# Kernel tuning notes

Hardware: AMD Instinct MI355X
Metric: run time of the kernel (lower is better)

Reference implementation:

```python
import jax, jax.numpy as jnp
import numpy as np

E = 128          # embedding_dim
H = 128          # decoder_hidden_dim
N = 200000       # number of candidate nodes


def setup_inputs() -> dict:
    key = jax.random.key(0)
    k0, k1, k2, k3, k4, k5 = jax.random.split(key, 6)
    return {
        "current_node_emb": jax.random.normal(k0, (1, E), jnp.float32),
        "context_emb": jax.random.normal(k1, (1, E), jnp.float32),
        "candidate_node_embs": jax.random.normal(k2, (N, E), jnp.float32),
        "Wq": jax.random.normal(k3, (H, 2 * E), jnp.float32) * 0.05,  # nn.Linear(2E->H, bias=False) weight
        "Wk": jax.random.normal(k4, (H, E), jnp.float32) * 0.05,      # nn.Linear(E->H, bias=False) weight
        "mask": jax.random.randint(k5, (1, N), 0, 2, jnp.int32),
    }


def reference(current_node_emb, context_emb, candidate_node_embs, Wq, Wk, mask):
    # combined_input = cat([current, context], dim=1) -> [1, 2E]
    combined = jnp.concatenate([current_node_emb, context_emb], axis=1)
    query = combined @ Wq.T                      # [1, H]
    keys = candidate_node_embs @ Wk.T            # [N, H]
    attn_scores = query @ keys.T                 # [1, N]
    masked = jnp.where(mask == 0, -jnp.inf, attn_scores)
    probs = jax.nn.softmax(masked, axis=1)       # [1, N]

    n = probs.shape[1]
    k = min(50, max(1, int(0.5 * n)))            # static Python int -> jit-friendly
    top_probs, _ = jax.lax.top_k(probs, k)       # [1, k]
    threshold = top_probs[:, -1:]                # [1, 1]
    top_mask = probs >= threshold
    filtered = probs * top_mask
    filtered = filtered / (jnp.sum(filtered, axis=1, keepdims=True) + 1e-10)

    log_probs_all = jnp.log(filtered + 1e-10)    # [1, N]
    # Categorical(filtered): true-zero probability outside top-k
    logits = jnp.where(filtered > 0, jnp.log(filtered), -jnp.inf)
    action_idx = jax.random.categorical(jax.random.key(42), logits, axis=1)  # [1]
    log_prob_action = jnp.take_along_axis(logits, action_idx[:, None], axis=1)[:, 0]  # [1]
    return (log_probs_all, log_prob_action, action_idx)
```

## Files before the change

### kernel.cpp

```cpp
#include <hip/hip_runtime.h>
#include <math.h>


#define CAP 4096
#define MAXB 128
#define NEG_INF (-__builtin_inff())

__device__ __forceinline__ unsigned int f2ord(float f){
  unsigned int b = __float_as_uint(f);
  return (b & 0x80000000u) ? ~b : (b | 0x80000000u);
}
__device__ __forceinline__ unsigned int rotl32(unsigned int x, int d){
  return (x << d) | (x >> (32 - d));
}

__device__ float gumbel_from_idx(unsigned int idx){
  unsigned int x0 = 0u, x1 = idx;
  const unsigned int ks0 = 0u, ks1 = 42u;
  const unsigned int ks2 = 0u ^ 42u ^ 0x1BD11BDAu;
  x0 += ks0; x1 += ks1;
#define TF_RND(r) { x0 += x1; x1 = rotl32(x1, (r)); x1 ^= x0; }
  TF_RND(13) TF_RND(15) TF_RND(26) TF_RND(6)
  x0 += ks1; x1 += ks2 + 1u;
  TF_RND(17) TF_RND(29) TF_RND(16) TF_RND(24)
  x0 += ks2; x1 += ks0 + 2u;
  TF_RND(13) TF_RND(15) TF_RND(26) TF_RND(6)
  x0 += ks0; x1 += ks1 + 3u;
  TF_RND(17) TF_RND(29) TF_RND(16) TF_RND(24)
  x0 += ks1; x1 += ks2 + 4u;
  TF_RND(13) TF_RND(15) TF_RND(26) TF_RND(6)
  x0 += ks2; x1 += ks0 + 5u;
#undef TF_RND
  unsigned int bits = x0 ^ x1;
  unsigned int fb = (bits >> 9) | 0x3f800000u;
  float f = __uint_as_float(fb) - 1.0f;
  float u = (f < 1.17549435e-38f) ? 1.17549435e-38f : f;
  return -logf(-logf(u));
}

__global__ __launch_bounds__(256) void k_prep(const float* __restrict__ cur,
    const float* __restrict__ ctx, const float* __restrict__ Wq,
    const float* __restrict__ Wk, float* __restrict__ v,
    unsigned int* __restrict__ hist, unsigned int* __restrict__ scal_u){
  __shared__ float q[128];
  __shared__ float vpart[256];
  int t = threadIdx.x;
  int lane = t & 63, wave = t >> 6;
  int hl = lane & 31, hi = lane >> 5;
  for (int k = t; k < 2048; k += 256) hist[k] = 0u;
  if (t < 16) scal_u[t] = 0u;
  float4 cb0 = ((const float4*)cur)[hl];
  float4 cb1 = ((const float4*)ctx)[hl];
  const float4* Wq4 = (const float4*)Wq;
  #pragma unroll 4
  for (int i = 0; i < 16; ++i){
    int row = wave * 32 + 2 * i + hi;
    float4 w0 = Wq4[row * 64 + hl];
    float4 w1 = Wq4[row * 64 + 32 + hl];
    float d = fmaf(w0.x, cb0.x, fmaf(w0.y, cb0.y, fmaf(w0.z, cb0.z, w0.w * cb0.w)));
    d = fmaf(w1.x, cb1.x, fmaf(w1.y, cb1.y, fmaf(w1.z, cb1.z, fmaf(w1.w, cb1.w, d))));
    d += __shfl_xor(d, 1, 64);
    d += __shfl_xor(d, 2, 64);
    d += __shfl_xor(d, 4, 64);
    d += __shfl_xor(d, 8, 64);
    d += __shfl_xor(d, 16, 64);
    if (hl == 0) q[row] = d;
  }
  __syncthreads();
  int col = t & 127, half = t >> 7;
  const float* wkp = Wk + half * 64 * 128 + col;
  const float* qp  = q + half * 64;
  float acc = 0.f;
  #pragma unroll 8
  for (int h = 0; h < 64; ++h) acc = fmaf(qp[h], wkp[h * 128], acc);
  vpart[t] = acc;
  __syncthreads();
  if (t < 128) v[t] = vpart[t] + vpart[t + 128];
}

__global__ __launch_bounds__(256) void k_score(const float* __restrict__ cand,
    const int* __restrict__ mask, const float* __restrict__ v,
    float* __restrict__ scores, float* __restrict__ out, int N){
  const float NLOG = logf(1e-10f);
  int t = threadIdx.x;
  int lane = t & 63, wave = t >> 6;
  int hi = lane >> 5, hl = lane & 31;
  float4 v4 = ((const float4*)v)[hl];
  const float4* cp = (const float4*)cand;
  int base = (blockIdx.x * 4 + wave) * 16;
  int m[8];
  #pragma unroll
  for (int k = 0; k < 8; ++k){
    int r = base + 2 * k + hi;
    r = (r < N) ? r : (N - 1);
    m[k] = mask[r];
  }
  float4 c[8];
  #pragma unroll
  for (int k = 0; k < 8; ++k){
    int r = base + 2 * k + hi;
    r = (r < N) ? r : (N - 1);
    c[k] = make_float4(0.f, 0.f, 0.f, 0.f);
    if (m[k]) c[k] = cp[(size_t)r * 32 + hl];
  }
  float p[8];
  #pragma unroll
  for (int k = 0; k < 8; ++k)
    p[k] = fmaf(c[k].x, v4.x, fmaf(c[k].y, v4.y, fmaf(c[k].z, v4.z, c[k].w * v4.w)));
  #pragma unroll
  for (int k = 0; k < 8; ++k){
    p[k] += __shfl_xor(p[k], 1, 64);
    p[k] += __shfl_xor(p[k], 2, 64);
    p[k] += __shfl_xor(p[k], 4, 64);
    p[k] += __shfl_xor(p[k], 8, 64);
    p[k] += __shfl_xor(p[k], 16, 64);
  }
  float sv = p[0];
  #pragma unroll
  for (int k = 1; k < 8; ++k) sv = (hl == k) ? p[k] : sv;
  if (hl < 8){
    int r = base + 2 * hl + hi;
    int mm = (hl < 8) ? ((hl == 0) ? m[0] : 0) : 0; (void)mm;
    if (r < N) scores[r] = mask[r] ? sv : NEG_INF;
  }
  if (t < 16){
    int o4 = blockIdx.x * 16 + t;
    if (o4 * 4 + 3 < N){
      ((float4*)out)[o4] = make_float4(NLOG, NLOG, NLOG, NLOG);
    } else {
      #pragma unroll
      for (int e = 0; e < 4; ++e){ int i = o4 * 4 + e; if (i < N) out[i] = NLOG; }
    }
  }
}

__global__ __launch_bounds__(1024) void k_tail(const float* __restrict__ scores,
    unsigned int* __restrict__ scal_u, unsigned int* __restrict__ hist,
    float* __restrict__ zpart, unsigned int* __restrict__ cnt,
    unsigned int* __restrict__ buf_idx, float* __restrict__ buf_s,
    float* __restrict__ out, int N, int ktop, int nb){
  __shared__ float sch[4096];
  __shared__ unsigned int lh[2048];
  __shared__ unsigned int ich[4096];
  __shared__ unsigned int suf[256];
  __shared__ unsigned int cnt_l[MAXB], offs[MAXB];
  __shared__ float wred[16];
  __shared__ float rv[16], rl[16];
  __shared__ unsigned int ri[16];
  __shared__ float Z_sh, thr_sh, lnD_sh;
  __shared__ unsigned int u_lo_sh;
  __shared__ int csel_sh, pos_sh, C_sh;
  int t = threadIdx.x, b = blockIdx.x;
  int lane = t & 63, wave = t >> 6;
  for (int k = t; k < 2048; k += 1024) lh[k] = 0u;
  if (t == 0) pos_sh = 0;
  __syncthreads();
  int base = b * 4096;
  float ez = 0.f;
  {
    int i0 = base + 4 * t;
    float4 s4 = make_float4(NEG_INF, NEG_INF, NEG_INF, NEG_INF);
    if (i0 + 3 < N) s4 = ((const float4*)scores)[(base >> 2) + t];
    else {
      if (i0     < N) s4.x = scores[i0];
      if (i0 + 1 < N) s4.y = scores[i0 + 1];
      if (i0 + 2 < N) s4.z = scores[i0 + 2];
      if (i0 + 3 < N) s4.w = scores[i0 + 3];
    }
    sch[4 * t]     = s4.x;
    sch[4 * t + 1] = s4.y;
    sch[4 * t + 2] = s4.z;
    sch[4 * t + 3] = s4.w;
#define HVISIT(s_) { float sx = (s_); if (sx > NEG_INF){ \
    atomicAdd(&lh[f2ord(sx) >> 21], 1u); ez += expf(sx); } }
    HVISIT(s4.x) HVISIT(s4.y) HVISIT(s4.z) HVISIT(s4.w)
#undef HVISIT
  }
  #pragma unroll
  for (int off = 32; off; off >>= 1) ez += __shfl_xor(ez, off, 64);
  if (lane == 0) wred[wave] = ez;
  __syncthreads();
  for (int k = t; k < 2048; k += 1024){
    unsigned int cc = lh[k];
    if (cc) atomicAdd(&hist[k], cc);
  }
  __syncthreads();
  if (t == 0){
    float z = 0.f;
    for (int w = 0; w < 16; ++w) z += wred[w];
    zpart[b] = z;
    __threadfence();
    atomicAdd(&scal_u[8], 1u);
  }
  if (b == 0){
    if (t == 0){
      while (__hip_atomic_load(&scal_u[8], __ATOMIC_ACQUIRE, __HIP_MEMORY_SCOPE_AGENT)
             < (unsigned)nb) __builtin_amdgcn_s_sleep(2);
      csel_sh = -1;
    }
    __syncthreads();
    float z = (t < nb) ? zpart[t] : 0.f;
    if (t < 128){
      #pragma unroll
      for (int off = 32; off; off >>= 1) z += __shfl_xor(z, off, 64);
      if (lane == 0) wred[wave] = z;
    }
    if (t < 256){
      unsigned int csum = 0;
      #pragma unroll
      for (int k = 0; k < 8; ++k) csum += hist[t * 8 + k];
      suf[t] = csum;
    }
    __syncthreads();
    if (t == 0) Z_sh = wred[0] + wred[1];
    for (int d = 1; d < 256; d <<= 1){
      unsigned int add = 0u;
      if (t < 256 && t + d < 256) add = suf[t + d];
      __syncthreads();
      if (t < 256) suf[t] += add;
      __syncthreads();
    }
    if (t < 256){
      unsigned int st = suf[t];
      unsigned int sn = (t < 255) ? suf[t + 1] : 0u;
      if (st >= (unsigned)ktop && sn < (unsigned)ktop) csel_sh = t;
    }
    __syncthreads();
    if (t == 0){
      int b_sel = 0;
      if (csel_sh >= 0){
        int c = csel_sh;
        unsigned int cum = (c < 255) ? suf[c + 1] : 0u;
        for (int bi = 8 * c + 7; bi >= 8 * c; --bi){
          cum += hist[bi];
          if (cum >= (unsigned)ktop){ b_sel = bi; break; }
        }
      }
      u_lo_sh = ((unsigned int)b_sel) << 21;
      scal_u[5] = u_lo_sh;
      __threadfence();
      __hip_atomic_store(&scal_u[9], 1u, __ATOMIC_RELEASE, __HIP_MEMORY_SCOPE_AGENT);
    }
    __syncthreads();
  } else {
    if (t == 0){
      while (__hip_atomic_load(&scal_u[9], __ATOMIC_ACQUIRE, __HIP_MEMORY_SCOPE_AGENT)
             == 0u) __builtin_amdgcn_s_sleep(2);
      u_lo_sh = scal_u[5];
    }
    __syncthreads();
  }
  unsigned int u_lo = u_lo_sh;
  for (int j = t; j < 4096; j += 1024){
    float sx = sch[j];
    if (sx > NEG_INF && f2ord(sx) >= u_lo){
      int p = atomicAdd(&pos_sh, 1);
      if (p < 4096){
        buf_s[b * 4096 + p] = sx;
        buf_idx[b * 4096 + p] = (unsigned int)(base + j);
      }
    }
  }
  __syncthreads();
  if (t == 0){
    cnt[b] = (unsigned int)((pos_sh > 4096) ? 4096 : pos_sh);
    __threadfence();
    atomicAdd(&scal_u[10], 1u);
  }
  if (b != 0) return;
  if (t == 0){
    while (__hip_atomic_load(&scal_u[10], __ATOMIC_ACQUIRE, __HIP_MEMORY_SCOPE_AGENT)
           < (unsigned)nb) __builtin_amdgcn_s_sleep(2);
  }
  __syncthreads();
  float* s_lds = sch;
  unsigned int* i_lds = ich;
  if (t < nb) cnt_l[t] = cnt[t];
  if (t == 0) thr_sh = NEG_INF;
  __syncthreads();
  if (t == 0){
    unsigned int acc = 0;
    for (int b2 = 0; b2 < nb; ++b2){ offs[b2] = acc; acc += cnt_l[b2]; }
    C_sh = (acc > CAP) ? CAP : (int)acc;
  }
  __syncthreads();
  for (int b2 = 0; b2 < nb; ++b2){
    unsigned int cb = cnt_l[b2], ob = offs[b2];
    for (unsigned int j = t; j < cb; j += 1024){
      unsigned int p = ob + j;
      if (p < CAP){ s_lds[p] = buf_s[b2 * 4096 + j]; i_lds[p] = buf_idx[b2 * 4096 + j]; }
    }
  }
  __syncthreads();
  int C = C_sh;
  if (C > ktop){
    for (int j = t; j < C; j += 1024){
      float sj = s_lds[j];
      int g = 0, e = 0;
      for (int k2 = 0; k2 < C; ++k2){
        float sk = s_lds[k2];
        g += (sk > sj);
        e += (sk == sj);
      }
      if (g < ktop && g + e >= ktop) thr_sh = sj;
    }
  }
  __syncthreads();
  float s_thr = thr_sh;
  float part = 0.f;
  for (int j = t; j < C; j += 1024){
    float sj = s_lds[j];
    if (sj >= s_thr) part += expf(sj);
  }
  #pragma unroll
  for (int off = 32; off; off >>= 1) part += __shfl_xor(part, off, 64);
  if (lane == 0) wred[wave] = part;
  __syncthreads();
  if (t == 0){
    float T = 0.f;
    for (int w = 0; w < 16; ++w) T += wred[w];
    lnD_sh = logf(T + 1e-10f * Z_sh);
  }
  __syncthreads();
  float lnD = lnD_sh;
  for (int j = t; j < C; j += 1024){
    float sj = s_lds[j];
    if (sj >= s_thr) out[i_lds[j]] = logf(expf(sj - lnD) + 1e-10f);
  }
  float bestv = NEG_INF, bestlogit = NEG_INF;
  unsigned int bestidx = 0xFFFFFFFFu;
  for (int j = t; j < C; j += 1024){
    float sj = s_lds[j];
    if (sj >= s_thr){
      unsigned int idx = i_lds[j];
      float logit = sj - lnD;
      float val = logit + gumbel_from_idx(idx);
      if (val > bestv || (val == bestv && idx < bestidx)){
        bestv = val; bestlogit = logit; bestidx = idx;
      }
    }
  }
  #pragma unroll
  for (int off = 32; off; off >>= 1){
    float ov = __shfl_xor(bestv, off, 64);
    float ol = __shfl_xor(bestlogit, off, 64);
    unsigned int oi = (unsigned int)__shfl_xor((int)bestidx, off, 64);
    if (ov > bestv || (ov == bestv && oi < bestidx)){
      bestv = ov; bestlogit = ol; bestidx = oi;
    }
  }
  if (lane == 0){ rv[wave] = bestv; rl[wave] = bestlogit; ri[wave] = bestidx; }
  __syncthreads();
  if (t == 0){
    for (int w = 1; w < 16; ++w){
      if (rv[w] > rv[0] || (rv[w] == rv[0] && ri[w] < ri[0])){
        rv[0] = rv[w]; rl[0] = rl[w]; ri[0] = ri[w];
      }
    }
    out[N] = rl[0];
    out[N + 1] = (float)ri[0];
  }
}

extern "C" void kernel_launch(void* const* d_in, const int* in_sizes, int n_in,
                              void* d_out, int out_size, void* d_ws, size_t ws_size,
                              hipStream_t stream){
  const float* cur  = (const float*)d_in[0];
  const float* ctx  = (const float*)d_in[1];
  const float* cand = (const float*)d_in[2];
  const float* Wq   = (const float*)d_in[3];
  const float* Wk   = (const float*)d_in[4];
  const int*   mask = (const int*)d_in[5];
  int N = in_sizes[5];
  float* out = (float*)d_out;

  char* ws = (char*)d_ws;
  unsigned int* scal_u  = (unsigned int*)ws;
  float*        v       = (float*)(ws + 512);
  float*        zpart   = (float*)(ws + 1024);
  unsigned int* cnt     = (unsigned int*)(ws + 1536);
  unsigned int* hist    = (unsigned int*)(ws + 4096);
  float*        scores  = (float*)(ws + 16384);
  char*         bufbase = ws + 16384 + (((size_t)N * 4 + 255) & ~255ull);
  float*        buf_s   = (float*)bufbase;
  unsigned int* buf_idx = (unsigned int*)(bufbase + (size_t)MAXB * 4096 * 4);

  int ktop = N / 2; if (ktop < 1) ktop = 1; if (ktop > 50) ktop = 50;
  int g_score = (N + 63) / 64;
  int nb = (N + 4095) / 4096;
  if (nb > MAXB) nb = MAXB;

  k_prep<<<1, 256, 0, stream>>>(cur, ctx, Wq, Wk, v, hist, scal_u);
  k_score<<<g_score, 256, 0, stream>>>(cand, mask, v, scores, out, N);
  k_tail<<<nb, 1024, 0, stream>>>(scores, scal_u, hist, zpart, cnt,
                                  buf_idx, buf_s, out, N, ktop, nb);
}
```

Before: 220.8 us.

## Replace global histogram barrier with per-block selection and refined last-block filter

Each tail block now builds its own score histogram and keeps only its local top-k candidates. This removes the global histogram atomics and the two grid-wide spin-wait barriers. The last block to finish, found with an atomic counter, merges the per-block candidates and runs a second histogram pass to shrink the set before the quadratic rank-based threshold search. The scoring kernel now loads candidate rows unconditionally instead of waiting on the mask, which reads masked-out rows it previously skipped.

```diff
diff --git a/kernel.cpp b/kernel.cpp
--- a/kernel.cpp
+++ b/kernel.cpp
@@ -3,7 +3,9 @@
 
 
 #define CAP 4096
-#define MAXB 128
+#define SLOT 2048
+#define MAXB 64
+#define C2CAP 2048
 #define NEG_INF (-__builtin_inff())
 
 __device__ __forceinline__ unsigned int f2ord(float f){
@@ -38,16 +40,52 @@
   return -logf(-logf(u));
 }
 
+__device__ void hist_select(unsigned int* lh, unsigned int* suf, int* csel_sh,
+                            unsigned int* u_lo_sh, int ktop, int t){
+  if (t < 256){
+    unsigned int csum = 0;
+    #pragma unroll
+    for (int k = 0; k < 8; ++k) csum += lh[t * 8 + k];
+    suf[t] = csum;
+  }
+  __syncthreads();
+  for (int d = 1; d < 256; d <<= 1){
+    unsigned int add = 0u;
+    if (t < 256 && t + d < 256) add = suf[t + d];
+    __syncthreads();
+    if (t < 256) suf[t] += add;
+    __syncthreads();
+  }
+  if (t < 256){
+    unsigned int st = suf[t];
+    unsigned int sn = (t < 255) ? suf[t + 1] : 0u;
+    if (st >= (unsigned)ktop && sn < (unsigned)ktop) *csel_sh = t;
+  }
+  __syncthreads();
+  if (t == 0){
+    int b_sel = 0;
+    int c = *csel_sh;
+    if (c >= 0){
+      unsigned int cum = (c < 255) ? suf[c + 1] : 0u;
+      for (int bi = 8 * c + 7; bi >= 8 * c; --bi){
+        cum += lh[bi];
+        if (cum >= (unsigned)ktop){ b_sel = bi; break; }
+      }
+    }
+    *u_lo_sh = ((unsigned int)b_sel) << 21;
+  }
+  __syncthreads();
+}
+
 __global__ __launch_bounds__(256) void k_prep(const float* __restrict__ cur,
     const float* __restrict__ ctx, const float* __restrict__ Wq,
     const float* __restrict__ Wk, float* __restrict__ v,
-    unsigned int* __restrict__ hist, unsigned int* __restrict__ scal_u){
+    unsigned int* __restrict__ scal_u){
   __shared__ float q[128];
   __shared__ float vpart[256];
   int t = threadIdx.x;
   int lane = t & 63, wave = t >> 6;
   int hl = lane & 31, hi = lane >> 5;
-  for (int k = t; k < 2048; k += 256) hist[k] = 0u;
   if (t < 16) scal_u[t] = 0u;
   float4 cb0 = ((const float4*)cur)[hl];
   float4 cb1 = ((const float4*)ctx)[hl];
@@ -88,20 +126,12 @@
   float4 v4 = ((const float4*)v)[hl];
   const float4* cp = (const float4*)cand;
   int base = (blockIdx.x * 4 + wave) * 16;
-  int m[8];
+  float4 c[8];
   #pragma unroll
   for (int k = 0; k < 8; ++k){
     int r = base + 2 * k + hi;
     r = (r < N) ? r : (N - 1);
-    m[k] = mask[r];
-  }
-  float4 c[8];
-  #pragma unroll
-  for (int k = 0; k < 8; ++k){
-    int r = base + 2 * k + hi;
-    r = (r < N) ? r : (N - 1);
-    c[k] = make_float4(0.f, 0.f, 0.f, 0.f);
-    if (m[k]) c[k] = cp[(size_t)r * 32 + hl];
+    c[k] = cp[(size_t)r * 32 + hl];
   }
   float p[8];
   #pragma unroll
@@ -120,7 +150,6 @@
   for (int k = 1; k < 8; ++k) sv = (hl == k) ? p[k] : sv;
   if (hl < 8){
     int r = base + 2 * hl + hi;
-    int mm = (hl < 8) ? ((hl == 0) ? m[0] : 0) : 0; (void)mm;
     if (r < N) scores[r] = mask[r] ? sv : NEG_INF;
   }
   if (t < 16){
@@ -135,25 +164,27 @@
 }
 
 __global__ __launch_bounds__(1024) void k_tail(const float* __restrict__ scores,
-    unsigned int* __restrict__ scal_u, unsigned int* __restrict__ hist,
-    float* __restrict__ zpart, unsigned int* __restrict__ cnt,
-    unsigned int* __restrict__ buf_idx, float* __restrict__ buf_s,
-    float* __restrict__ out, int N, int ktop, int nb){
+    unsigned int* __restrict__ scal_u, float* __restrict__ zpart,
+    unsigned int* __restrict__ cnt, unsigned int* __restrict__ buf_idx,
+    float* __restrict__ buf_s, float* __restrict__ out,
+    int N, int ktop, int nb){
   __shared__ float sch[4096];
+  __shared__ unsigned int ich[4096];
   __shared__ unsigned int lh[2048];
-  __shared__ unsigned int ich[4096];
   __shared__ unsigned int suf[256];
+  __shared__ float s2[C2CAP];
+  __shared__ unsigned int i2[C2CAP];
   __shared__ unsigned int cnt_l[MAXB], offs[MAXB];
   __shared__ float wred[16];
   __shared__ float rv[16], rl[16];
   __shared__ unsigned int ri[16];
   __shared__ float Z_sh, thr_sh, lnD_sh;
   __shared__ unsigned int u_lo_sh;
-  __shared__ int csel_sh, pos_sh, C_sh;
+  __shared__ int csel_sh, pos_sh, C_sh, last_sh;
   int t = threadIdx.x, b = blockIdx.x;
   int lane = t & 63, wave = t >> 6;
   for (int k = t; k < 2048; k += 1024) lh[k] = 0u;
-  if (t == 0) pos_sh = 0;
+  if (t == 0){ pos_sh = 0; csel_sh = -1; }
   __syncthreads();
   int base = b * 4096;
   float ez = 0.f;
@@ -165,7 +196,6 @@
       if (i0     < N) s4.x = scores[i0];
       if (i0 + 1 < N) s4.y = scores[i0 + 1];
       if (i0 + 2 < N) s4.z = scores[i0 + 2];
-      if (i0 + 3 < N) s4.w = scores[i0 + 3];
     }
     sch[4 * t]     = s4.x;
     sch[4 * t + 1] = s4.y;
@@ -180,103 +210,41 @@
   for (int off = 32; off; off >>= 1) ez += __shfl_xor(ez, off, 64);
   if (lane == 0) wred[wave] = ez;
   __syncthreads();
-  for (int k = t; k < 2048; k += 1024){
-    unsigned int cc = lh[k];
-    if (cc) atomicAdd(&hist[k], cc);
-  }
-  __syncthreads();
-  if (t == 0){
-    float z = 0.f;
-    for (int w = 0; w < 16; ++w) z += wred[w];
-    zpart[b] = z;
-    __threadfence();
-    atomicAdd(&scal_u[8], 1u);
-  }
-  if (b == 0){
-    if (t == 0){
-      while (__hip_atomic_load(&scal_u[8], __ATOMIC_ACQUIRE, __HIP_MEMORY_SCOPE_AGENT)
-             < (unsigned)nb) __builtin_amdgcn_s_sleep(2);
-      csel_sh = -1;
-    }
-    __syncthreads();
-    float z = (t < nb) ? zpart[t] : 0.f;
-    if (t < 128){
-      #pragma unroll
-      for (int off = 32; off; off >>= 1) z += __shfl_xor(z, off, 64);
-      if (lane == 0) wred[wave] = z;
-    }
-    if (t < 256){
-      unsigned int csum = 0;
-      #pragma unroll
-      for (int k = 0; k < 8; ++k) csum += hist[t * 8 + k];
-      suf[t] = csum;
-    }
-    __syncthreads();
-    if (t == 0) Z_sh = wred[0] + wred[1];
-    for (int d = 1; d < 256; d <<= 1){
-      unsigned int add = 0u;
-      if (t < 256 && t + d < 256) add = suf[t + d];
-      __syncthreads();
-      if (t < 256) suf[t] += add;
-      __syncthreads();
-    }
-    if (t < 256){
-      unsigned int st = suf[t];
-      unsigned int sn = (t < 255) ? suf[t + 1] : 0u;
-      if (st >= (unsigned)ktop && sn < (unsigned)ktop) csel_sh = t;
-    }
-    __syncthreads();
-    if (t == 0){
-      int b_sel = 0;
-      if (csel_sh >= 0){
-        int c = csel_sh;
-        unsigned int cum = (c < 255) ? suf[c + 1] : 0u;
-        for (int bi = 8 * c + 7; bi >= 8 * c; --bi){
-          cum += hist[bi];
-          if (cum >= (unsigned)ktop){ b_sel = bi; break; }
-        }
-      }
-      u_lo_sh = ((unsigned int)b_sel) << 21;
-      scal_u[5] = u_lo_sh;
-      __threadfence();
-      __hip_atomic_store(&scal_u[9], 1u, __ATOMIC_RELEASE, __HIP_MEMORY_SCOPE_AGENT);
-    }
-    __syncthreads();
-  } else {
-    if (t == 0){
-      while (__hip_atomic_load(&scal_u[9], __ATOMIC_ACQUIRE, __HIP_MEMORY_SCOPE_AGENT)
-             == 0u) __builtin_amdgcn_s_sleep(2);
-      u_lo_sh = scal_u[5];
-    }
-    __syncthreads();
-  }
+  hist_select(lh, suf, &csel_sh, &u_lo_sh, ktop, t);
   unsigned int u_lo = u_lo_sh;
   for (int j = t; j < 4096; j += 1024){
     float sx = sch[j];
     if (sx > NEG_INF && f2ord(sx) >= u_lo){
       int p = atomicAdd(&pos_sh, 1);
-      if (p < 4096){
-        buf_s[b * 4096 + p] = sx;
-        buf_idx[b * 4096 + p] = (unsigned int)(base + j);
-      }
-    }
-  }
-  __syncthreads();
-  if (t == 0){
-    cnt[b] = (unsigned int)((pos_sh > 4096) ? 4096 : pos_sh);
+      if (p < SLOT){
+        buf_s[(size_t)b * SLOT + p] = sx;
+        buf_idx[(size_t)b * SLOT + p] = (unsigned int)(base + j);
+      }
+    }
+  }
+  __syncthreads();
+  if (t == 0){
+    cnt[b] = (unsigned int)((pos_sh > SLOT) ? SLOT : pos_sh);
+    float z = 0.f;
+    for (int w = 0; w < 16; ++w) z += wred[w];
+    zpart[b] = z;
     __threadfence();
-    atomicAdd(&scal_u[10], 1u);
-  }
-  if (b != 0) return;
-  if (t == 0){
-    while (__hip_atomic_load(&scal_u[10], __ATOMIC_ACQUIRE, __HIP_MEMORY_SCOPE_AGENT)
-           < (unsigned)nb) __builtin_amdgcn_s_sleep(2);
-  }
-  __syncthreads();
-  float* s_lds = sch;
-  unsigned int* i_lds = ich;
+    unsigned int old = atomicAdd(&scal_u[8], 1u);
+    last_sh = (old == (unsigned)(nb - 1));
+  }
+  __syncthreads();
+  if (!last_sh) return;
+  __threadfence();
   if (t < nb) cnt_l[t] = cnt[t];
-  if (t == 0) thr_sh = NEG_INF;
+  {
+    float z = 0.f;
+    if (t < 64){
+      z = (t < nb) ? zpart[t] : 0.f;
+      #pragma unroll
+      for (int off = 32; off; off >>= 1) z += __shfl_xor(z, off, 64);
+    }
+    if (t == 0){ Z_sh = z; thr_sh = NEG_INF; pos_sh = 0; csel_sh = -1; }
+  }
   __syncthreads();
   if (t == 0){
     unsigned int acc = 0;
@@ -288,17 +256,34 @@
     unsigned int cb = cnt_l[b2], ob = offs[b2];
     for (unsigned int j = t; j < cb; j += 1024){
       unsigned int p = ob + j;
-      if (p < CAP){ s_lds[p] = buf_s[b2 * 4096 + j]; i_lds[p] = buf_idx[b2 * 4096 + j]; }
-    }
-  }
+      if (p < CAP){
+        sch[p] = buf_s[(size_t)b2 * SLOT + j];
+        ich[p] = buf_idx[(size_t)b2 * SLOT + j];
+      }
+    }
+  }
+  for (int k = t; k < 2048; k += 1024) lh[k] = 0u;
   __syncthreads();
   int C = C_sh;
-  if (C > ktop){
-    for (int j = t; j < C; j += 1024){
-      float sj = s_lds[j];
+  for (int j = t; j < C; j += 1024) atomicAdd(&lh[f2ord(sch[j]) >> 21], 1u);
+  __syncthreads();
+  hist_select(lh, suf, &csel_sh, &u_lo_sh, ktop, t);
+  unsigned int u_lo2 = u_lo_sh;
+  for (int j = t; j < C; j += 1024){
+    float sx = sch[j];
+    if (f2ord(sx) >= u_lo2){
+      int p = atomicAdd(&pos_sh, 1);
+      if (p < C2CAP){ s2[p] = sx; i2[p] = ich[j]; }
+    }
+  }
+  __syncthreads();
+  int C2 = (pos_sh > C2CAP) ? C2CAP : pos_sh;
+  if (C2 > ktop){
+    for (int j = t; j < C2; j += 1024){
+      float sj = s2[j];
       int g = 0, e = 0;
-      for (int k2 = 0; k2 < C; ++k2){
-        float sk = s_lds[k2];
+      for (int k2 = 0; k2 < C2; ++k2){
+        float sk = s2[k2];
         g += (sk > sj);
         e += (sk == sj);
       }
@@ -308,8 +293,8 @@
   __syncthreads();
   float s_thr = thr_sh;
   float part = 0.f;
-  for (int j = t; j < C; j += 1024){
-    float sj = s_lds[j];
+  for (int j = t; j < C2; j += 1024){
+    float sj = s2[j];
     if (sj >= s_thr) part += expf(sj);
   }
   #pragma unroll
@@ -323,16 +308,16 @@
   }
   __syncthreads();
   float lnD = lnD_sh;
-  for (int j = t; j < C; j += 1024){
-    float sj = s_lds[j];
-    if (sj >= s_thr) out[i_lds[j]] = logf(expf(sj - lnD) + 1e-10f);
+  for (int j = t; j < C2; j += 1024){
+    float sj = s2[j];
+    if (sj >= s_thr) out[i2[j]] = logf(expf(sj - lnD) + 1e-10f);
   }
   float bestv = NEG_INF, bestlogit = NEG_INF;
   unsigned int bestidx = 0xFFFFFFFFu;
-  for (int j = t; j < C; j += 1024){
-    float sj = s_lds[j];
+  for (int j = t; j < C2; j += 1024){
+    float sj = s2[j];
     if (sj >= s_thr){
-      unsigned int idx = i_lds[j];
+      unsigned int idx = i2[j];
       float logit = sj - lnD;
       float val = logit + gumbel_from_idx(idx);
       if (val > bestv || (val == bestv && idx < bestidx)){
@@ -379,19 +364,18 @@
   float*        v       = (float*)(ws + 512);
   float*        zpart   = (float*)(ws + 1024);
   unsigned int* cnt     = (unsigned int*)(ws + 1536);
-  unsigned int* hist    = (unsigned int*)(ws + 4096);
-  float*        scores  = (float*)(ws + 16384);
-  char*         bufbase = ws + 16384 + (((size_t)N * 4 + 255) & ~255ull);
+  float*        scores  = (float*)(ws + 4096);
+  char*         bufbase = ws + 4096 + (((size_t)N * 4 + 255) & ~255ull);
   float*        buf_s   = (float*)bufbase;
-  unsigned int* buf_idx = (unsigned int*)(bufbase + (size_t)MAXB * 4096 * 4);
+  unsigned int* buf_idx = (unsigned int*)(bufbase + (size_t)MAXB * SLOT * 4);
 
   int ktop = N / 2; if (ktop < 1) ktop = 1; if (ktop > 50) ktop = 50;
   int g_score = (N + 63) / 64;
   int nb = (N + 4095) / 4096;
   if (nb > MAXB) nb = MAXB;
 
-  k_prep<<<1, 256, 0, stream>>>(cur, ctx, Wq, Wk, v, hist, scal_u);
+  k_prep<<<1, 256, 0, stream>>>(cur, ctx, Wq, Wk, v, scal_u);
   k_score<<<g_score, 256, 0, stream>>>(cand, mask, v, scores, out, N);
-  k_tail<<<nb, 1024, 0, stream>>>(scores, scal_u, hist, zpart, cnt,
+  k_tail<<<nb, 1024, 0, stream>>>(scores, scal_u, zpart, cnt,
                                   buf_idx, buf_s, out, N, ktop, nb);
 }
```

Measured after the change: 220.3 us. No clear change (-0.2%).
